# Performance work log

Measured on AMD Instinct MI355X. Metric: run time of the kernel, lower is better.

The kernel has to match this reference:

```python
import jax, jax.numpy as jnp
import numpy as np
import math

B, S, D, H, R = 4, 2048, 2048, 16, 16
HD = D // H

def setup_inputs() -> dict:
    key = jax.random.key(0)
    ks = jax.random.split(key, 16)
    x = jax.random.normal(ks[0], (B, S, D), dtype=jnp.float32)
    # causal mask: 1 where attendable, 0 where masked (mask==0 -> -1e9)
    mask = jnp.tril(jnp.ones((S, S), dtype=jnp.int32))[None, None, :, :]
    def lin(k):
        return jax.random.normal(k, (D, D), dtype=jnp.float32) / math.sqrt(D)
    def lora(ka, kb):
        A = jax.random.normal(ka, (R, D), dtype=jnp.float32) / math.sqrt(D)
        Bm = jnp.zeros((D, R), dtype=jnp.float32)  # standard LoRA init: B = 0
        return A, Bm
    Aq, Bq = lora(ks[1], ks[2]); Ak, Bk = lora(ks[3], ks[4])
    Av, Bv = lora(ks[5], ks[6]); Ao, Bo = lora(ks[7], ks[8])
    return {"x": x, "mask": mask,
            "Wq": lin(ks[9]), "Aq": Aq, "Bq": Bq,
            "Wk": lin(ks[10]), "Ak": Ak, "Bk": Bk,
            "Wv": lin(ks[11]), "Av": Av, "Bv": Bv,
            "Wo": lin(ks[12]), "Ao": Ao, "Bo": Bo}

def _lora_linear(x, W, A, Bm):
    # y = x @ W^T + (x @ A^T) @ B^T   (LoRA-augmented linear, no bias)
    return x @ W.T + (x @ A.T) @ Bm.T

def reference(x, mask, Wq, Aq, Bq, Wk, Ak, Bk, Wv, Av, Bv, Wo, Ao, Bo):
    b, s, d = x.shape
    def heads(t):
        return t.reshape(b, s, H, HD).transpose(0, 2, 1, 3)  # [B,H,S,HD]
    Q = heads(_lora_linear(x, Wq, Aq, Bq))
    K = heads(_lora_linear(x, Wk, Ak, Bk))
    V = heads(_lora_linear(x, Wv, Av, Bv))
    attn = jnp.einsum('bhqd,bhkd->bhqk', Q, K) / math.sqrt(HD)
    attn = jnp.where(mask == 0, jnp.float32(-1e9), attn)
    attn = jax.nn.softmax(attn, axis=-1)
    out = jnp.einsum('bhqk,bhkd->bhqd', attn, V)  # [B,H,S,HD]
    out = out.transpose(0, 2, 1, 3).reshape(b, s, d)
    return _lora_linear(out, Wo, Ao, Bo)
```

## Files before the change

### kernel.cpp

```cpp
#include <hip/hip_runtime.h>
#include <hip/hip_bf16.h>
#include <stdint.h>


#define L2E 1.4426950408889634f
#define SMSCALE 0.08838834764831845f
#define NEGBIG -3.0e38f

typedef __attribute__((ext_vector_type(4))) float f32x4;
typedef __attribute__((ext_vector_type(16))) float f32x16;
typedef __attribute__((ext_vector_type(8))) __bf16 bfrag;

#if __has_builtin(__builtin_amdgcn_exp2f)
#define EXP2 __builtin_amdgcn_exp2f
#else
#define EXP2 exp2f
#endif

#define DRAIN_VM                                      \
  do {                                                \
    asm volatile("s_waitcnt vmcnt(0)" ::: "memory");  \
    __builtin_amdgcn_sched_barrier(0);                \
  } while (0)

static __device__ __forceinline__ unsigned short f2bf(float f) {
  union { float f; unsigned u; } v; v.f = f;
  unsigned r = v.u + 0x7FFFu + ((v.u >> 16) & 1u);
  return (unsigned short)(r >> 16);
}

static __device__ __forceinline__ void gload16(const void* g, void* l) {
  __builtin_amdgcn_global_load_lds(
      (const __attribute__((address_space(1))) void*)g,
      (__attribute__((address_space(3))) void*)l, 16, 0, 0);
}

__global__ __launch_bounds__(256) void k_fold(const float* __restrict__ W,
                                              const float* __restrict__ A,
                                              const float* __restrict__ Bm,
                                              unsigned short* __restrict__ out) {
  const int n = blockIdx.x;
  const int k0 = threadIdx.x * 8;
  const float* wr = W + (size_t)n * 2048 + k0;
  float acc[8];
#pragma unroll
  for (int j = 0; j < 8; ++j) acc[j] = wr[j];
#pragma unroll 4
  for (int r = 0; r < 16; ++r) {
    float b = Bm[n * 16 + r];
    const float* ar = A + (size_t)r * 2048 + k0;
#pragma unroll
    for (int j = 0; j < 8; ++j) acc[j] = fmaf(b, ar[j], acc[j]);
  }
  unsigned short o[8];
#pragma unroll
  for (int j = 0; j < 8; ++j) o[j] = f2bf(acc[j]);
  *(uint4*)(out + (size_t)n * 2048 + k0) = *(const uint4*)o;
}

__global__ __launch_bounds__(256) void k_cvt(const float* __restrict__ in,
                                             unsigned short* __restrict__ out) {
  const size_t i = ((size_t)blockIdx.x * 256 + threadIdx.x) * 8;
  unsigned short o[8];
#pragma unroll
  for (int j = 0; j < 8; ++j) o[j] = f2bf(in[i + j]);
  *(uint4*)(out + i) = *(const uint4*)o;
}

template <int MODE>
__global__ __launch_bounds__(256) void k_gemm(const unsigned short* __restrict__ A,
                                              const unsigned short* __restrict__ Bw,
                                              void* __restrict__ Cout, float scale) {
  constexpr int Kd = 2048, Nd = 2048;
  __shared__ unsigned short Asm[128 * 64];
  __shared__ unsigned short Bsm[128 * 64];
  const int tid = threadIdx.x, ln = tid & 63, w = tid >> 6;
  const int wm = w >> 1, wn = w & 1, g = ln >> 4, cc = ln & 15;
  const int m0 = blockIdx.y * 128, n0 = blockIdx.x * 128;

  f32x4 acc[4][4] = {};

  for (int kt = 0; kt < Kd; kt += 64) {
#pragma unroll
    for (int i = 0; i < 4; ++i) {
      int cid = i * 256 + tid;
      int row = cid >> 3, ch = cid & 7;
      int sch = ch ^ (row & 7);
      gload16(A + (size_t)(m0 + row) * Kd + kt + sch * 8,
              (char*)Asm + cid * 16);
      gload16(Bw + (size_t)(n0 + row) * Kd + kt + sch * 8,
              (char*)Bsm + cid * 16);
    }
    __syncthreads();
#pragma unroll
    for (int s = 0; s < 2; ++s) {
      bfrag af[4], bfr[4];
#pragma unroll
      for (int fm = 0; fm < 4; ++fm) {
        int row = wm * 64 + fm * 16 + cc;
        int o = s * 64 + g * 16;
        af[fm] = *(const bfrag*)((const char*)Asm + row * 128 + (o ^ ((row & 7) << 4)));
      }
#pragma unroll
      for (int fn = 0; fn < 4; ++fn) {
        int row = wn * 64 + fn * 16 + cc;
        int o = s * 64 + g * 16;
        bfr[fn] = *(const bfrag*)((const char*)Bsm + row * 128 + (o ^ ((row & 7) << 4)));
      }
#pragma unroll
      for (int fm = 0; fm < 4; ++fm)
#pragma unroll
        for (int fn = 0; fn < 4; ++fn)
          acc[fm][fn] = __builtin_amdgcn_mfma_f32_16x16x32_bf16(af[fm], bfr[fn],
                                                                acc[fm][fn], 0, 0, 0);
    }
    __syncthreads();
  }

#pragma unroll
  for (int fm = 0; fm < 4; ++fm)
#pragma unroll
    for (int fn = 0; fn < 4; ++fn)
#pragma unroll
      for (int r = 0; r < 4; ++r) {
        int row = m0 + wm * 64 + fm * 16 + g * 4 + r;
        int col = n0 + wn * 64 + fn * 16 + cc;
        float v = acc[fm][fn][r];
        if (MODE == 0) {
          int b = row >> 11, s = row & 2047, h = col >> 7, hd = col & 127;
          ((unsigned short*)Cout)[(((size_t)b * 16 + h) * 2048 + s) * 128 + hd] =
              f2bf(v * scale);
        } else if (MODE == 2) {
          int b = row >> 11, s = row & 2047, h = col >> 7, hd = col & 127;
          ((unsigned short*)Cout)[(((size_t)b * 16 + h) * 128 + hd) * 2048 + s] =
              f2bf(v);
        } else {
          ((float*)Cout)[(size_t)row * Nd + col] = v;
        }
      }
}

__global__ __launch_bounds__(512) void k_attn(const unsigned short* __restrict__ Q,
                                              const unsigned short* __restrict__ K,
                                              const unsigned short* __restrict__ Vt,
                                              unsigned short* __restrict__ O) {
  __shared__ __align__(16) unsigned char lds[65536];
  const int tid = threadIdx.x;
  const int ln = tid & 63, w = tid >> 6;
  const int l31 = ln & 31, hi = ln >> 5;
  const int rk = l31 & 15;
  const int bx = blockIdx.x;
  const int qb = 7 - (bx >> 6);
  const int bh = bx & 63;
  const int q0 = qb * 256;
  const size_t base = (size_t)bh * 2048 * 128;
  const unsigned short* Qb = Q + base;
  const unsigned short* Kb = K + base;
  const unsigned short* Vb = Vt + base;

  const int qw0 = q0 + w * 32;
  const int qg = qw0 + l31;

  bfrag qf[8];
#pragma unroll
  for (int dc = 0; dc < 8; ++dc)
    qf[dc] = *(const bfrag*)(Qb + (size_t)qg * 128 + dc * 16 + hi * 8);

  f32x16 o[4] = {};
  float m_r = NEGBIG, l_r = 0.f;

  const int nt = q0 / 64 + 4;

  auto stage = [&](int buf, int k0) {
    unsigned char* Kt = lds + buf * 32768;
    unsigned char* Vl = Kt + 16384;
#pragma unroll
    for (int i = 0; i < 2; ++i) {
      int cid = i * 512 + tid;
      int row = cid >> 4, p = cid & 15, sc = p ^ (row & 15);
      gload16(Kb + (size_t)(k0 + row) * 128 + sc * 8, Kt + cid * 16);
    }
#pragma unroll
    for (int i = 0; i < 2; ++i) {
      int cid = i * 512 + tid;
      int row = cid >> 4, p = cid & 15, sc = p ^ (row & 15);
      int d = (sc >> 3) * 64 + row;
      gload16(Vb + (size_t)d * 2048 + k0 + (sc & 7) * 8, Vl + cid * 16);
    }
  };

  stage(0, 0);
  DRAIN_VM;
  __syncthreads();
  int buf = 0;

  for (int t = 0; t < nt; ++t) {
    const int k0 = t * 64;
    if (t + 1 < nt) stage(buf ^ 1, k0 + 64);

    if (k0 <= qw0 + 31) {
      const unsigned char* Kt = lds + buf * 32768;
      const unsigned char* Vl = Kt + 16384;

      f32x16 s0 = {}, s1 = {};
#pragma unroll
      for (int dc = 0; dc < 8; ++dc) {
        int c = dc * 2 + hi;
        bfrag ka = *(const bfrag*)(Kt + (size_t)l31 * 256 + ((c ^ rk) << 4));
        bfrag kb2 = *(const bfrag*)(Kt + (size_t)(32 + l31) * 256 + ((c ^ rk) << 4));
        s0 = __builtin_amdgcn_mfma_f32_32x32x16_bf16(ka, qf[dc], s0, 0, 0, 0);
        s1 = __builtin_amdgcn_mfma_f32_32x32x16_bf16(kb2, qf[dc], s1, 0, 0, 0);
      }

      if (k0 + 63 > qw0) {
#pragma unroll
        for (int r = 0; r < 16; ++r) {
          int ko = (r & 3) + 8 * (r >> 2) + 4 * hi;
          if (k0 + ko > qg) s0[r] = NEGBIG;
          if (k0 + 32 + ko > qg) s1[r] = NEGBIG;
        }
      }

      float pmax = s0[0];
#pragma unroll
      for (int r = 1; r < 16; ++r) pmax = fmaxf(pmax, s0[r]);
#pragma unroll
      for (int r = 0; r < 16; ++r) pmax = fmaxf(pmax, s1[r]);
      pmax = fmaxf(pmax, __shfl_xor(pmax, 32));

      if (!__all(pmax - m_r <= 12.f)) {
        float mn = fmaxf(m_r, pmax);
        float al = EXP2(m_r - mn);
        l_r *= al;
#pragma unroll
        for (int db = 0; db < 4; ++db)
#pragma unroll
          for (int r = 0; r < 16; ++r) o[db][r] *= al;
        m_r = mn;
      }

      unsigned qd0[8], qd1[8];
      float rs = 0.f;
#pragma unroll
      for (int s = 0; s < 4; ++s) {
        float p0 = EXP2(s0[4 * s + 0] - m_r), p1 = EXP2(s0[4 * s + 1] - m_r);
        float p2 = EXP2(s0[4 * s + 2] - m_r), p3 = EXP2(s0[4 * s + 3] - m_r);
        rs += (p0 + p1) + (p2 + p3);
        qd0[2 * s] = (unsigned)f2bf(p0) | ((unsigned)f2bf(p1) << 16);
        qd0[2 * s + 1] = (unsigned)f2bf(p2) | ((unsigned)f2bf(p3) << 16);
      }
#pragma unroll
      for (int s = 0; s < 4; ++s) {
        float p0 = EXP2(s1[4 * s + 0] - m_r), p1 = EXP2(s1[4 * s + 1] - m_r);
        float p2 = EXP2(s1[4 * s + 2] - m_r), p3 = EXP2(s1[4 * s + 3] - m_r);
        rs += (p0 + p1) + (p2 + p3);
        qd1[2 * s] = (unsigned)f2bf(p0) | ((unsigned)f2bf(p1) << 16);
        qd1[2 * s + 1] = (unsigned)f2bf(p2) | ((unsigned)f2bf(p3) << 16);
      }
      rs += __shfl_xor(rs, 32);
      l_r += rs;

#define PVSTEP(QD, B0, KC)                                                    \
  do {                                                                        \
    unsigned e0 = QD[B0], e1 = QD[B0 + 1], x0 = QD[B0 + 2], x1 = QD[B0 + 3];  \
    unsigned kp0 = hi ? x0 : e0, kp1 = hi ? x1 : e1;                          \
    unsigned sd0 = hi ? e0 : x0, sd1 = hi ? e1 : x1;                          \
    unsigned rc0 = (unsigned)__shfl_xor((int)sd0, 32);                        \
    unsigned rc1 = (unsigned)__shfl_xor((int)sd1, 32);                        \
    unsigned pw[4];                                                           \
    pw[0] = hi ? rc0 : kp0; pw[1] = hi ? rc1 : kp1;                           \
    pw[2] = hi ? kp0 : rc0; pw[3] = hi ? kp1 : rc1;                           \
    bfrag pf = *(bfrag*)pw;                                                   \
    _Pragma("unroll")                                                         \
    for (int db = 0; db < 4; ++db) {                                          \
      int c = (db >> 1) * 8 + KC * 2 + hi;                                    \
      bfrag vf = *(const bfrag*)(Vl + (size_t)((db & 1) * 32 + l31) * 256 +   \
                                 ((c ^ rk) << 4));                            \
      o[db] = __builtin_amdgcn_mfma_f32_32x32x16_bf16(vf, pf, o[db], 0, 0, 0);\
    }                                                                         \
  } while (0)

      PVSTEP(qd0, 0, 0);
      PVSTEP(qd0, 4, 1);
      PVSTEP(qd1, 0, 2);
      PVSTEP(qd1, 4, 3);
#undef PVSTEP
    }
    DRAIN_VM;
    __syncthreads();
    buf ^= 1;
  }

  float invl = 1.0f / l_r;
  const int b_ = bh >> 4, h_ = bh & 15;
#pragma unroll
  for (int ph = 0; ph < 2; ++ph) {
    if ((w >> 2) == ph) {
      unsigned char* ep = lds + (w & 3) * 8704;
#pragma unroll
      for (int db = 0; db < 4; ++db)
#pragma unroll
        for (int s = 0; s < 4; ++s) {
          int d0 = db * 32 + 8 * s + 4 * hi;
          float v0 = o[db][4 * s] * invl, v1 = o[db][4 * s + 1] * invl;
          float v2 = o[db][4 * s + 2] * invl, v3 = o[db][4 * s + 3] * invl;
          uint2 pw;
          pw.x = (unsigned)f2bf(v0) | ((unsigned)f2bf(v1) << 16);
          pw.y = (unsigned)f2bf(v2) | ((unsigned)f2bf(v3) << 16);
          *(uint2*)(ep + l31 * 272 + d0 * 2) = pw;
        }
    }
    __syncthreads();
    if ((w >> 2) == ph) {
      const unsigned char* ep = lds + (w & 3) * 8704;
#pragma unroll
      for (int i = 0; i < 8; ++i) {
        int cid = i * 64 + ln;
        int q = cid >> 4, ch = cid & 15;
        uint4 val = *(const uint4*)(ep + q * 272 + ch * 16);
        *(uint4*)(O + ((size_t)(b_ * 2048 + q0 + w * 32 + q)) * 2048 +
                  h_ * 128 + ch * 8) = val;
      }
    }
    __syncthreads();
  }
}

extern "C" void kernel_launch(void* const* d_in, const int* in_sizes, int n_in,
                              void* d_out, int out_size, void* d_ws, size_t ws_size,
                              hipStream_t stream) {
  (void)in_sizes; (void)n_in; (void)out_size; (void)ws_size;
  const float* x  = (const float*)d_in[0];
  const float* Wq = (const float*)d_in[2];
  const float* Aq = (const float*)d_in[3];
  const float* Bq = (const float*)d_in[4];
  const float* Wk = (const float*)d_in[5];
  const float* Ak = (const float*)d_in[6];
  const float* Bk = (const float*)d_in[7];
  const float* Wv = (const float*)d_in[8];
  const float* Av = (const float*)d_in[9];
  const float* Bv = (const float*)d_in[10];
  const float* Wo = (const float*)d_in[11];
  const float* Ao = (const float*)d_in[12];
  const float* Bo = (const float*)d_in[13];

  char* ws = (char*)d_ws;
  unsigned short* xbf = (unsigned short*)ws;
  unsigned short* Wqe = (unsigned short*)(ws + (size_t)33554432);
  unsigned short* Wke = Wqe + 2048 * 2048;
  unsigned short* Wve = Wke + 2048 * 2048;
  unsigned short* Woe = Wve + 2048 * 2048;
  unsigned short* Qb  = (unsigned short*)(ws + (size_t)33554432 + 4u * 8388608u);
  unsigned short* Kb  = Qb + 16777216;
  unsigned short* Vtb = Kb + 16777216;
  unsigned short* AO  = xbf;

  k_fold<<<2048, 256, 0, stream>>>(Wq, Aq, Bq, Wqe);
  k_fold<<<2048, 256, 0, stream>>>(Wk, Ak, Bk, Wke);
  k_fold<<<2048, 256, 0, stream>>>(Wv, Av, Bv, Wve);
  k_fold<<<2048, 256, 0, stream>>>(Wo, Ao, Bo, Woe);
  k_cvt<<<8192, 256, 0, stream>>>(x, xbf);

  dim3 gg(16, 64);
  k_gemm<0><<<gg, 256, 0, stream>>>(xbf, Wqe, Qb, SMSCALE * L2E);
  k_gemm<0><<<gg, 256, 0, stream>>>(xbf, Wke, Kb, 1.0f);
  k_gemm<2><<<gg, 256, 0, stream>>>(xbf, Wve, Vtb, 1.0f);

  k_attn<<<512, 512, 0, stream>>>(Qb, Kb, Vtb, AO);

  k_gemm<1><<<gg, 256, 0, stream>>>(AO, Woe, d_out, 1.0f);
}
```

Measured before the change: 505.2 us.

## Replace GEMM with 256x256 double-buffered pipelined kernel and rebalance attention order

The 128x128 single-buffered GEMM is replaced by a 512-thread 256x256 tile kernel. It double-buffers LDS (128KB), prefetches the next K tile in halves between MFMA groups, uses a new XOR swizzle, raises wave priority around MFMAs and remaps blocks for L2 locality. It aims to hide global-load latency and raise operand reuse per block. The attention block order also changes so the second half of blocks processes query tiles in ascending order, balancing causal work. The trade-offs are higher LDS and register pressure and only 256 blocks per GEMM.

New measurement: 422.3 us. 16.4% less time.

```diff
diff --git a/kernel.cpp b/kernel.cpp
--- a/kernel.cpp
+++ b/kernel.cpp
@@ -68,62 +68,118 @@
 }
 
 template <int MODE>
-__global__ __launch_bounds__(256) void k_gemm(const unsigned short* __restrict__ A,
-                                              const unsigned short* __restrict__ Bw,
-                                              void* __restrict__ Cout, float scale) {
-  constexpr int Kd = 2048, Nd = 2048;
-  __shared__ unsigned short Asm[128 * 64];
-  __shared__ unsigned short Bsm[128 * 64];
-  const int tid = threadIdx.x, ln = tid & 63, w = tid >> 6;
-  const int wm = w >> 1, wn = w & 1, g = ln >> 4, cc = ln & 15;
-  const int m0 = blockIdx.y * 128, n0 = blockIdx.x * 128;
-
-  f32x4 acc[4][4] = {};
-
-  for (int kt = 0; kt < Kd; kt += 64) {
-#pragma unroll
-    for (int i = 0; i < 4; ++i) {
-      int cid = i * 256 + tid;
-      int row = cid >> 3, ch = cid & 7;
-      int sch = ch ^ (row & 7);
-      gload16(A + (size_t)(m0 + row) * Kd + kt + sch * 8,
-              (char*)Asm + cid * 16);
-      gload16(Bw + (size_t)(n0 + row) * Kd + kt + sch * 8,
-              (char*)Bsm + cid * 16);
-    }
-    __syncthreads();
-#pragma unroll
-    for (int s = 0; s < 2; ++s) {
-      bfrag af[4], bfr[4];
-#pragma unroll
-      for (int fm = 0; fm < 4; ++fm) {
-        int row = wm * 64 + fm * 16 + cc;
-        int o = s * 64 + g * 16;
-        af[fm] = *(const bfrag*)((const char*)Asm + row * 128 + (o ^ ((row & 7) << 4)));
-      }
-#pragma unroll
-      for (int fn = 0; fn < 4; ++fn) {
-        int row = wn * 64 + fn * 16 + cc;
-        int o = s * 64 + g * 16;
-        bfr[fn] = *(const bfrag*)((const char*)Bsm + row * 128 + (o ^ ((row & 7) << 4)));
-      }
-#pragma unroll
-      for (int fm = 0; fm < 4; ++fm)
-#pragma unroll
-        for (int fn = 0; fn < 4; ++fn)
-          acc[fm][fn] = __builtin_amdgcn_mfma_f32_16x16x32_bf16(af[fm], bfr[fn],
-                                                                acc[fm][fn], 0, 0, 0);
-    }
-    __syncthreads();
-  }
-
-#pragma unroll
-  for (int fm = 0; fm < 4; ++fm)
+__global__ __launch_bounds__(512, 2) void k_gemm2(const unsigned short* __restrict__ A,
+                                                  const unsigned short* __restrict__ Bw,
+                                                  void* __restrict__ Cout, float scale) {
+  __shared__ __align__(16) unsigned char lds[131072];
+  unsigned char* Al = lds;
+  unsigned char* Bl = lds + 65536;
+  const int tid = threadIdx.x, ln = tid & 63;
+  const int w = tid >> 6, g = ln >> 4, cc = ln & 15;
+  const int wm = w >> 2, wn = w & 3;
+  const int bid = blockIdx.x;
+  const int wg = (bid & 7) * 32 + (bid >> 3);
+  const int m0 = (wg >> 3) * 256, n0 = (wg & 7) * 256;
+
+  int soff[2], sdst[2];
+#pragma unroll
+  for (int i = 0; i < 2; ++i) {
+    int cid = i * 512 + tid, r = cid >> 2, p = cid & 3;
+    int sc = p ^ ((r >> 1) & 3);
+    soff[i] = r * 2048 + sc * 8;
+    sdst[i] = cid * 16;
+  }
+  int aro[8], bro[4];
+#pragma unroll
+  for (int fm = 0; fm < 8; ++fm) {
+    int r = wm * 128 + fm * 16 + cc;
+    aro[fm] = r * 64 + ((g ^ ((r >> 1) & 3)) << 4);
+  }
+#pragma unroll
+  for (int fn = 0; fn < 4; ++fn) {
+    int r = wn * 64 + fn * 16 + cc;
+    bro[fn] = r * 64 + ((g ^ ((r >> 1) & 3)) << 4);
+  }
+
+#define STAGE_A(b, kt, h)                                                   \
+  do {                                                                      \
+    _Pragma("unroll")                                                       \
+    for (int i = 0; i < 2; ++i)                                             \
+      gload16(A + (size_t)m0 * 2048 + soff[i] + (kt) + (h) * 32,            \
+              Al + (b) * 32768 + (h) * 16384 + sdst[i]);                    \
+  } while (0)
+#define STAGE_B(b, kt, h)                                                   \
+  do {                                                                      \
+    _Pragma("unroll")                                                       \
+    for (int i = 0; i < 2; ++i)                                             \
+      gload16(Bw + (size_t)n0 * 2048 + soff[i] + (kt) + (h) * 32,           \
+              Bl + (b) * 32768 + (h) * 16384 + sdst[i]);                    \
+  } while (0)
+
+  f32x4 acc[8][4] = {};
+
+  STAGE_A(0, 0, 0); STAGE_B(0, 0, 0); STAGE_A(0, 0, 1); STAGE_B(0, 0, 1);
+  asm volatile("s_waitcnt vmcnt(4)" ::: "memory");
+  __builtin_amdgcn_s_barrier();
+  __builtin_amdgcn_sched_barrier(0);
+
+  for (int T = 0; T < 32; ++T) {
+    const int buf = T & 1;
+    const unsigned char* Ab = Al + buf * 32768;
+    const unsigned char* Bb = Bl + buf * 32768;
+    const int ktn = (T + 1) * 64;
+    const bool pf = (T + 1 < 32);
+#pragma unroll
+    for (int ks = 0; ks < 2; ++ks) {
+      bfrag af[8], bf[4];
+#pragma unroll
+      for (int fm = 0; fm < 8; ++fm)
+        af[fm] = *(const bfrag*)(Ab + ks * 16384 + aro[fm]);
+#pragma unroll
+      for (int j = 0; j < 2; ++j)
+        bf[j] = *(const bfrag*)(Bb + ks * 16384 + bro[j]);
+      if (pf) STAGE_A(buf ^ 1, ktn, ks);
+      __builtin_amdgcn_sched_barrier(0);
+      __builtin_amdgcn_s_barrier();
+      __builtin_amdgcn_sched_barrier(0);
+      __builtin_amdgcn_s_setprio(1);
+#pragma unroll
+      for (int fm = 0; fm < 8; ++fm)
+#pragma unroll
+        for (int j = 0; j < 2; ++j)
+          acc[fm][j] = __builtin_amdgcn_mfma_f32_16x16x32_bf16(af[fm], bf[j],
+                                                               acc[fm][j], 0, 0, 0);
+      __builtin_amdgcn_s_setprio(0);
+      __builtin_amdgcn_sched_barrier(0);
+#pragma unroll
+      for (int j = 0; j < 2; ++j)
+        bf[2 + j] = *(const bfrag*)(Bb + ks * 16384 + bro[2 + j]);
+      if (pf) STAGE_B(buf ^ 1, ktn, ks);
+      __builtin_amdgcn_sched_barrier(0);
+      asm volatile("s_waitcnt vmcnt(4)" ::: "memory");
+      __builtin_amdgcn_s_barrier();
+      __builtin_amdgcn_sched_barrier(0);
+      __builtin_amdgcn_s_setprio(1);
+#pragma unroll
+      for (int fm = 0; fm < 8; ++fm)
+#pragma unroll
+        for (int j = 0; j < 2; ++j)
+          acc[fm][2 + j] = __builtin_amdgcn_mfma_f32_16x16x32_bf16(af[fm], bf[2 + j],
+                                                                   acc[fm][2 + j], 0, 0, 0);
+      __builtin_amdgcn_s_setprio(0);
+      __builtin_amdgcn_sched_barrier(0);
+    }
+  }
+#undef STAGE_A
+#undef STAGE_B
+
+#pragma unroll
+  for (int fm = 0; fm < 8; ++fm)
 #pragma unroll
     for (int fn = 0; fn < 4; ++fn)
 #pragma unroll
       for (int r = 0; r < 4; ++r) {
-        int row = m0 + wm * 64 + fm * 16 + g * 4 + r;
+        int row = m0 + wm * 128 + fm * 16 + g * 4 + r;
         int col = n0 + wn * 64 + fn * 16 + cc;
         float v = acc[fm][fn][r];
         if (MODE == 0) {
@@ -135,7 +191,7 @@
           ((unsigned short*)Cout)[(((size_t)b * 16 + h) * 128 + hd) * 2048 + s] =
               f2bf(v);
         } else {
-          ((float*)Cout)[(size_t)row * Nd + col] = v;
+          ((float*)Cout)[(size_t)row * 2048 + col] = v;
         }
       }
 }
@@ -150,7 +206,8 @@
   const int l31 = ln & 31, hi = ln >> 5;
   const int rk = l31 & 15;
   const int bx = blockIdx.x;
-  const int qb = 7 - (bx >> 6);
+  const int gqb = bx >> 6;
+  const int qb = (bx < 256) ? (7 - gqb) : (gqb - 4);
   const int bh = bx & 63;
   const int q0 = qb * 256;
   const size_t base = (size_t)bh * 2048 * 128;
@@ -361,12 +418,11 @@
   k_fold<<<2048, 256, 0, stream>>>(Wo, Ao, Bo, Woe);
   k_cvt<<<8192, 256, 0, stream>>>(x, xbf);
 
-  dim3 gg(16, 64);
-  k_gemm<0><<<gg, 256, 0, stream>>>(xbf, Wqe, Qb, SMSCALE * L2E);
-  k_gemm<0><<<gg, 256, 0, stream>>>(xbf, Wke, Kb, 1.0f);
-  k_gemm<2><<<gg, 256, 0, stream>>>(xbf, Wve, Vtb, 1.0f);
+  k_gemm2<0><<<256, 512, 0, stream>>>(xbf, Wqe, Qb, SMSCALE * L2E);
+  k_gemm2<0><<<256, 512, 0, stream>>>(xbf, Wke, Kb, 1.0f);
+  k_gemm2<2><<<256, 512, 0, stream>>>(xbf, Wve, Vtb, 1.0f);
 
   k_attn<<<512, 512, 0, stream>>>(Qb, Kb, Vtb, AO);
 
-  k_gemm<1><<<gg, 256, 0, stream>>>(AO, Woe, d_out, 1.0f);
-}
+  k_gemm2<1><<<256, 512, 0, stream>>>(AO, Woe, d_out, 1.0f);
+}
```
